# Optimization experiments

Measured on AMD Instinct MI355X. Metric: run time of the kernel, lower is better.

The kernel has to match this reference:

```python
import jax, jax.numpy as jnp
import numpy as np

N = 100000
E = 1600000
IN_C = 512
OUT_C = 128


def setup_inputs() -> dict:
    key = jax.random.key(0)
    k1, k2, k3, k4 = jax.random.split(key, 4)
    x = jax.random.normal(k1, (N, IN_C), dtype=jnp.float32)
    edge_index = jax.random.randint(k2, (2, E), 0, N, dtype=jnp.int64)
    # GCNConv parameters (glorot weight, zero bias as in PyG defaults)
    scale = jnp.sqrt(6.0 / (IN_C + OUT_C)).astype(jnp.float32)
    W = jax.random.uniform(k3, (IN_C, OUT_C), dtype=jnp.float32, minval=-scale, maxval=scale)
    b = jnp.zeros((OUT_C,), dtype=jnp.float32)
    return {"x": x, "edge_index": edge_index, "W": W, "b": b}


def reference(x, edge_index, W, b):
    n = x.shape[0]
    loops = jnp.arange(n, dtype=edge_index.dtype)
    src = jnp.concatenate([edge_index[0], loops])  # [E+N] message sources
    dst = jnp.concatenate([edge_index[1], loops])  # [E+N] message targets
    # symmetric GCN normalization: deg over targets incl. self-loops
    deg = jax.ops.segment_sum(jnp.ones_like(src, dtype=x.dtype), dst, num_segments=n)
    dinv = jnp.where(deg > 0, jax.lax.rsqrt(deg), 0.0)
    norm = dinv[src] * dinv[dst]  # [E+N]
    h = x @ W  # [N, OUT_C] transform first (in > out)
    msg = h[src] * norm[:, None]  # [E+N, OUT_C]
    out = jax.ops.segment_sum(msg, dst, num_segments=n) + b
    return (out, 0)
```

## Files before the change

kernel.cpp:

```cpp
#include <hip/hip_runtime.h>

#define IN_C 512
#define OUT_C 128
#define NB 128
#define CHUNK 16384

typedef float f32x4 __attribute__((ext_vector_type(4)));
typedef __bf16 bf16x8 __attribute__((ext_vector_type(8)));

static inline int cdiv(int a, int b) { return (a + b - 1) / b; }

__device__ __forceinline__ unsigned short bfbits(__bf16 h) {
  return __builtin_bit_cast(unsigned short, h);
}


__global__ __launch_bounds__(256) void hist_kernel(const int* __restrict__ dst,
                                                   int* __restrict__ table,
                                                   int nchunks, int E) {
  __shared__ int hcnt[NB];
  int t = threadIdx.x;
  int c = blockIdx.x;
  if (t < NB) hcnt[t] = 0;
  __syncthreads();
  int base = c * CHUNK;
  for (int i = t; i < CHUNK; i += 256) {
    int e = base + i;
    if (e < E) atomicAdd(&hcnt[dst[e] >> 10], 1);
  }
  __syncthreads();
  if (t < NB) table[t * nchunks + c] = hcnt[t];
}

__global__ __launch_bounds__(256) void tscan_kernel(int* __restrict__ table,
                                                    int* __restrict__ bstart,
                                                    int nchunks, int E) {
  __shared__ int sh[256];
  int t = threadIdx.x;
  int total = NB * nchunks;
  int S = (total + 255) / 256;
  int lo = t * S;
  int hi = lo + S; if (hi > total) hi = total;
  int s = 0;
  int i = lo;
  for (; i + 4 <= hi; i += 4)
    s += table[i] + table[i + 1] + table[i + 2] + table[i + 3];
  for (; i < hi; i++) s += table[i];
  sh[t] = s;
  __syncthreads();
  for (int off = 1; off < 256; off <<= 1) {
    int x = sh[t];
    if (t >= off) x += sh[t - off];
    __syncthreads();
    sh[t] = x;
    __syncthreads();
  }
  int run = sh[t] - s;
  for (i = lo; i < hi; i++) {
    int v = table[i];
    table[i] = run;
    run += v;
  }
  __syncthreads();
  for (int b = t; b < NB; b += 256) bstart[b] = table[b * nchunks];
  if (t == 0) bstart[NB] = E;
}

__global__ __launch_bounds__(256) void scat2_kernel(const int* __restrict__ src,
                                                    const int* __restrict__ dst,
                                                    const int* __restrict__ table,
                                                    int* __restrict__ inter,
                                                    int nchunks, int E) {
  __shared__ int cur[NB];
  int t = threadIdx.x;
  int c = blockIdx.x;
  if (t < NB) cur[t] = table[t * nchunks + c];
  __syncthreads();
  int base = c * CHUNK;
  for (int i = t; i < CHUNK; i += 256) {
    int e = base + i;
    if (e < E) {
      int d = dst[e];
      int pos = atomicAdd(&cur[d >> 10], 1);
      inter[pos] = (src[e] << 10) | (d & 1023);
    }
  }
}

__global__ __launch_bounds__(256) void bdeg_offs_kernel(const int* __restrict__ inter,
                                                        const int* __restrict__ bstart,
                                                        int* __restrict__ offs,
                                                        float* __restrict__ dinv,
                                                        int n, int E, int nbk) {
  __shared__ int dl[1024];
  __shared__ int sh[256];
  int t = threadIdx.x;
  int b = blockIdx.x;
  for (int i = t; i < 1024; i += 256) dl[i] = 0;
  __syncthreads();
  int lo = bstart[b], hi = bstart[b + 1];
  for (int e = lo + t; e < hi; e += 256) atomicAdd(&dl[inter[e] & 1023], 1);
  __syncthreads();
  int c[4];
  int s = 0;
#pragma unroll
  for (int j = 0; j < 4; j++) {
    c[j] = dl[t * 4 + j];
    s += c[j];
  }
  sh[t] = s;
  __syncthreads();
  for (int off = 1; off < 256; off <<= 1) {
    int x = sh[t];
    if (t >= off) x += sh[t - off];
    __syncthreads();
    sh[t] = x;
    __syncthreads();
  }
  int run = sh[t] - s + lo;
  int nb0 = b << 10;
#pragma unroll
  for (int j = 0; j < 4; j++) {
    int node = nb0 + t * 4 + j;
    if (node < n) {
      offs[node] = run;
      dinv[node] = rsqrtf((float)c[j] + 1.0f);
    }
    run += c[j];
  }
  if (b == nbk - 1 && t == 255) offs[n] = E;
}

__global__ __launch_bounds__(256) void scat3_kernel(const int* __restrict__ inter,
                                                    const int* __restrict__ bstart,
                                                    const int* __restrict__ offs,
                                                    int* __restrict__ csr_src, int n) {
  __shared__ int cur[1024];
  int t = threadIdx.x;
  int b = blockIdx.x;
  int nb0 = b << 10;
  for (int i = t; i < 1024; i += 256) {
    int node = nb0 + i;
    cur[i] = (node < n) ? offs[node] : 0;
  }
  __syncthreads();
  int lo = bstart[b], hi = bstart[b + 1];
  for (int e = lo + t; e < hi; e += 256) {
    int u = inter[e];
    int pos = atomicAdd(&cur[u & 1023], 1);
    csr_src[pos] = u >> 10;
  }
}

__global__ __launch_bounds__(256) void wsplit_kernel(const float* __restrict__ W,
                                                     unsigned short* __restrict__ wfh,
                                                     unsigned short* __restrict__ wfl) {
  int i = blockIdx.x * 256 + threadIdx.x;
  if (i >= IN_C * OUT_C) return;
  int k = i >> 7;
  int col = i & 127;
  float w = W[i];
  __bf16 hb = (__bf16)w;
  __bf16 lb = (__bf16)(w - (float)hb);
  int ks = k >> 5;
  int lg = (k & 31) >> 3;
  int j = k & 7;
  int cb = col >> 4;
  int lane = lg * 16 + (col & 15);
  size_t idx = ((size_t)(ks * 8 + cb) * 64 + lane) * 8 + j;
  wfh[idx] = bfbits(hb);
  wfl[idx] = bfbits(lb);
}

__global__ __launch_bounds__(256) void gemm_mfma_kernel(
    const float* __restrict__ x, const unsigned short* __restrict__ wfh,
    const unsigned short* __restrict__ wfl, const float* __restrict__ dinv,
    unsigned short* __restrict__ h, int n) {
  __shared__ float xs[2][4096];

  const int tid = threadIdx.x;
  const int wv = tid >> 6;
  const int lane = tid & 63;
  const int l15 = lane & 15;
  const int lg = lane >> 4;
  const int wr = wv >> 1;
  const int wc = wv & 1;
  const int row0 = blockIdx.x * 128;

  const float* gsrc[4];
#pragma unroll
  for (int i = 0; i < 4; i++) {
    int pslot = i * 256 + tid;
    int row = pslot >> 3;
    int q = pslot & 7;
    int s = q ^ (row & 7);
    int grow = row0 + row;
    if (grow > n - 1) grow = n - 1;
    gsrc[i] = x + (size_t)grow * IN_C + s * 4;
  }

  const unsigned short* bph = wfh + ((size_t)(wc * 4) * 64 + lane) * 8;
  const unsigned short* bpl = wfl + ((size_t)(wc * 4) * 64 + lane) * 8;

  f32x4 acc[4][4];
#pragma unroll
  for (int i = 0; i < 4; i++)
#pragma unroll
    for (int j = 0; j < 4; j++) acc[i][j] = (f32x4)0.0f;

#pragma unroll
  for (int i = 0; i < 4; i++) {
    char* lp = (char*)&xs[0][0] + i * 4096 + wv * 1024;
    __builtin_amdgcn_global_load_lds(
        (const __attribute__((address_space(1))) void*)gsrc[i],
        (__attribute__((address_space(3))) void*)lp, 16, 0, 0);
    gsrc[i] += 32;
  }

  for (int ks = 0; ks < 16; ks++) {
    __builtin_amdgcn_s_barrier();
    bf16x8 bh[4], bl[4];
#pragma unroll
    for (int nt = 0; nt < 4; nt++) {
      bh[nt] = __builtin_bit_cast(bf16x8, *(const uint4*)(bph + (size_t)ks * 4096 + nt * 512));
      bl[nt] = __builtin_bit_cast(bf16x8, *(const uint4*)(bpl + (size_t)ks * 4096 + nt * 512));
    }
    if (ks < 15) {
#pragma unroll
      for (int i = 0; i < 4; i++) {
        char* lp = (char*)&xs[(ks + 1) & 1][0] + i * 4096 + wv * 1024;
        __builtin_amdgcn_global_load_lds(
            (const __attribute__((address_space(1))) void*)gsrc[i],
            (__attribute__((address_space(3))) void*)lp, 16, 0, 0);
        gsrc[i] += 32;
      }
      asm volatile("s_waitcnt vmcnt(12)" ::: "memory");
    } else {
      asm volatile("s_waitcnt vmcnt(8)" ::: "memory");
    }
    __builtin_amdgcn_s_barrier();

    const float* bp = &xs[ks & 1][0];
    bf16x8 ah[4];
#pragma unroll
    for (int rt = 0; rt < 4; rt++) {
      int row = wr * 64 + rt * 16 + l15;
      int r7 = row & 7;
      int s0 = (lg * 2) ^ r7;
      int s1 = (lg * 2 + 1) ^ r7;
      float4 f0 = *(const float4*)(bp + row * 32 + s0 * 4);
      float4 f1 = *(const float4*)(bp + row * 32 + s1 * 4);
      float f[8] = {f0.x, f0.y, f0.z, f0.w, f1.x, f1.y, f1.z, f1.w};
      bf16x8 hh;
#pragma unroll
      for (int j = 0; j < 8; j++) hh[j] = (__bf16)f[j];
      ah[rt] = hh;
    }
#pragma unroll
    for (int rt = 0; rt < 4; rt++)
#pragma unroll
      for (int nt = 0; nt < 4; nt++) {
        acc[rt][nt] = __builtin_amdgcn_mfma_f32_16x16x32_bf16(ah[rt], bh[nt], acc[rt][nt], 0, 0, 0);
        acc[rt][nt] = __builtin_amdgcn_mfma_f32_16x16x32_bf16(ah[rt], bl[nt], acc[rt][nt], 0, 0, 0);
      }
  }

#pragma unroll
  for (int rt = 0; rt < 4; rt++) {
    int rowbase = row0 + wr * 64 + rt * 16 + lg * 4;
#pragma unroll
    for (int r = 0; r < 4; r++) {
      int row = rowbase + r;
      if (row < n) {
        float di = dinv[row];
#pragma unroll
        for (int nt = 0; nt < 4; nt++) {
          int col = wc * 64 + nt * 16 + l15;
          h[(size_t)row * OUT_C + col] = bfbits((__bf16)(acc[rt][nt][r] * di));
        }
      }
    }
  }
}

__device__ __forceinline__ float bflo(unsigned int u) {
  return __builtin_bit_cast(float, u << 16);
}
__device__ __forceinline__ float bfhi(unsigned int u) {
  return __builtin_bit_cast(float, u & 0xffff0000u);
}

__global__ __launch_bounds__(256) void gather_kernel(const int* __restrict__ offs,
                                                     const int* __restrict__ csr_src,
                                                     const unsigned short* __restrict__ h,
                                                     const float* __restrict__ dinv,
                                                     const float* __restrict__ b,
                                                     float* __restrict__ out,
                                                     int n, int tail) {
  int wid = threadIdx.x >> 6;
  int lane = threadIdx.x & 63;
  int l15 = lane & 15;
  int q = lane >> 4;
  int node = blockIdx.x * 4 + wid;
  if (node >= n) return;

  int start = offs[node];
  int end = offs[node + 1];

  float ax0 = 0, ay0 = 0, ax1 = 0, ay1 = 0, ax2 = 0, ay2 = 0, ax3 = 0, ay3 = 0;

  int e = start + q;
  for (; e + 12 < end; e += 16) {
    int s0 = csr_src[e];
    int s1 = csr_src[e + 4];
    int s2 = csr_src[e + 8];
    int s3 = csr_src[e + 12];
    uint4 u0 = *(const uint4*)(h + (size_t)s0 * OUT_C + l15 * 8);
    uint4 u1 = *(const uint4*)(h + (size_t)s1 * OUT_C + l15 * 8);
    uint4 u2 = *(const uint4*)(h + (size_t)s2 * OUT_C + l15 * 8);
    uint4 u3 = *(const uint4*)(h + (size_t)s3 * OUT_C + l15 * 8);
    ax0 += (bflo(u0.x) + bflo(u1.x)) + (bflo(u2.x) + bflo(u3.x));
    ay0 += (bfhi(u0.x) + bfhi(u1.x)) + (bfhi(u2.x) + bfhi(u3.x));
    ax1 += (bflo(u0.y) + bflo(u1.y)) + (bflo(u2.y) + bflo(u3.y));
    ay1 += (bfhi(u0.y) + bfhi(u1.y)) + (bfhi(u2.y) + bfhi(u3.y));
    ax2 += (bflo(u0.z) + bflo(u1.z)) + (bflo(u2.z) + bflo(u3.z));
    ay2 += (bfhi(u0.z) + bfhi(u1.z)) + (bfhi(u2.z) + bfhi(u3.z));
    ax3 += (bflo(u0.w) + bflo(u1.w)) + (bflo(u2.w) + bflo(u3.w));
    ay3 += (bfhi(u0.w) + bfhi(u1.w)) + (bfhi(u2.w) + bfhi(u3.w));
  }
  for (; e < end; e += 4) {
    int s0 = csr_src[e];
    uint4 u0 = *(const uint4*)(h + (size_t)s0 * OUT_C + l15 * 8);
    ax0 += bflo(u0.x); ay0 += bfhi(u0.x);
    ax1 += bflo(u0.y); ay1 += bfhi(u0.y);
    ax2 += bflo(u0.z); ay2 += bfhi(u0.z);
    ax3 += bflo(u0.w); ay3 += bfhi(u0.w);
  }

#pragma unroll
  for (int mask = 16; mask <= 32; mask <<= 1) {
    ax0 += __shfl_xor(ax0, mask); ay0 += __shfl_xor(ay0, mask);
    ax1 += __shfl_xor(ax1, mask); ay1 += __shfl_xor(ay1, mask);
    ax2 += __shfl_xor(ax2, mask); ay2 += __shfl_xor(ay2, mask);
    ax3 += __shfl_xor(ax3, mask); ay3 += __shfl_xor(ay3, mask);
  }

  float dd = dinv[node];
  uint4 us = *(const uint4*)(h + (size_t)node * OUT_C + l15 * 8);
  ax0 = (ax0 + bflo(us.x)) * dd; ay0 = (ay0 + bfhi(us.x)) * dd;
  ax1 = (ax1 + bflo(us.y)) * dd; ay1 = (ay1 + bfhi(us.y)) * dd;
  ax2 = (ax2 + bflo(us.z)) * dd; ay2 = (ay2 + bfhi(us.z)) * dd;
  ax3 = (ax3 + bflo(us.w)) * dd; ay3 = (ay3 + bfhi(us.w)) * dd;

  if (q == 0) {
    float4 b0 = *(const float4*)(b + l15 * 8);
    float4 b1 = *(const float4*)(b + l15 * 8 + 4);
    float4 o0 = make_float4(ax0 + b0.x, ay0 + b0.y, ax1 + b0.z, ay1 + b0.w);
    float4 o1 = make_float4(ax2 + b1.x, ay2 + b1.y, ax3 + b1.z, ay3 + b1.w);
    float* op = out + (size_t)node * OUT_C + l15 * 8;
    *(float4*)op = o0;
    *(float4*)(op + 4) = o1;
  }

  if (node == 0 && lane == 0) {
    for (int t = 0; t < tail; t++) out[(size_t)n * OUT_C + t] = 0.0f;
  }
}

extern "C" void kernel_launch(void* const* d_in, const int* in_sizes, int n_in,
                              void* d_out, int out_size, void* d_ws, size_t ws_size,
                              hipStream_t stream) {
  const float* x = (const float*)d_in[0];
  const int* ei = (const int*)d_in[1];
  const float* W = (const float*)d_in[2];
  const float* b = (const float*)d_in[3];

  const int n = in_sizes[0] / IN_C;
  const int E = in_sizes[1] / 2;
  const int* src = ei;
  const int* dst = ei + E;
  float* out = (float*)d_out;

  const int nchunks = cdiv(E, CHUNK);
  const int nbk = cdiv(n, 1024);

  size_t p = 0;
  auto alloc = [&](size_t bytes) { size_t o = p; p += (bytes + 255) & ~(size_t)255; return o; };
  char* ws = (char*)d_ws;
  float*          dinv   = (float*)(ws + alloc((size_t)n * 4));
  int*            offs   = (int*)(ws + alloc(((size_t)n + 1) * 4));
  int*            csrsrc = (int*)(ws + alloc((size_t)E * 4));
  int*            bstart = (int*)(ws + alloc((NB + 1) * 4));
  unsigned short* wfh    = (unsigned short*)(ws + alloc((size_t)IN_C * OUT_C * 2));
  unsigned short* wfl    = (unsigned short*)(ws + alloc((size_t)IN_C * OUT_C * 2));
  size_t upos = p;
  int*            inter  = (int*)(ws + upos);
  int*            table  = (int*)(ws + upos + (((size_t)E * 4 + 255) & ~(size_t)255));
  unsigned short* h      = (unsigned short*)(ws + upos);

  wsplit_kernel<<<cdiv(IN_C * OUT_C, 256), 256, 0, stream>>>(W, wfh, wfl);
  hist_kernel<<<nchunks, 256, 0, stream>>>(dst, table, nchunks, E);
  tscan_kernel<<<1, 256, 0, stream>>>(table, bstart, nchunks, E);
  scat2_kernel<<<nchunks, 256, 0, stream>>>(src, dst, table, inter, nchunks, E);
  bdeg_offs_kernel<<<nbk, 256, 0, stream>>>(inter, bstart, offs, dinv, n, E, nbk);
  scat3_kernel<<<nbk, 256, 0, stream>>>(inter, bstart, offs, csrsrc, n);
  gemm_mfma_kernel<<<cdiv(n, 128), 256, 0, stream>>>(x, wfh, wfl, dinv, h, n);
  int tail = out_size - n * OUT_C;
  gather_kernel<<<cdiv(n, 4), 256, 0, stream>>>(offs, csrsrc, h, dinv, b, out, n, tail);
}
```

Before: 281.3 us.

## Fuse bucket degree and CSR scatter kernels, simplify GEMM pipeline sync, halve chunk size

Merges the per-bucket degree/offset kernel with the CSR scatter kernel, so each bucket's running cursors stay in shared memory instead of being written to and reread from global memory, and one launch is dropped. Replaces the GEMM's explicit s_waitcnt/s_barrier double-buffer handshake with __syncthreads at the end of each k-step. This may serialize the prefetch more than the hand-tuned vmcnt waits did. Also halves CHUNK, which doubles the number of histogram/scatter blocks and enlarges the chunk table.

Result: faster. 264.7 us (-5.9%).

```diff
diff --git a/kernel.cpp b/kernel.cpp
--- a/kernel.cpp
+++ b/kernel.cpp
@@ -3,7 +3,7 @@
 #define IN_C 512
 #define OUT_C 128
 #define NB 128
-#define CHUNK 16384
+#define CHUNK 8192
 
 typedef float f32x4 __attribute__((ext_vector_type(4)));
 typedef __bf16 bf16x8 __attribute__((ext_vector_type(8)));
@@ -87,12 +87,14 @@
   }
 }
 
-__global__ __launch_bounds__(256) void bdeg_offs_kernel(const int* __restrict__ inter,
-                                                        const int* __restrict__ bstart,
-                                                        int* __restrict__ offs,
-                                                        float* __restrict__ dinv,
-                                                        int n, int E, int nbk) {
+__global__ __launch_bounds__(256) void bucket_csr_kernel(const int* __restrict__ inter,
+                                                         const int* __restrict__ bstart,
+                                                         int* __restrict__ offs,
+                                                         float* __restrict__ dinv,
+                                                         int* __restrict__ csr_src,
+                                                         int n, int E, int nbk) {
   __shared__ int dl[1024];
+  __shared__ int curs[1024];
   __shared__ int sh[256];
   int t = threadIdx.x;
   int b = blockIdx.x;
@@ -126,28 +128,14 @@
       offs[node] = run;
       dinv[node] = rsqrtf((float)c[j] + 1.0f);
     }
+    curs[t * 4 + j] = run;
     run += c[j];
   }
   if (b == nbk - 1 && t == 255) offs[n] = E;
-}
-
-__global__ __launch_bounds__(256) void scat3_kernel(const int* __restrict__ inter,
-                                                    const int* __restrict__ bstart,
-                                                    const int* __restrict__ offs,
-                                                    int* __restrict__ csr_src, int n) {
-  __shared__ int cur[1024];
-  int t = threadIdx.x;
-  int b = blockIdx.x;
-  int nb0 = b << 10;
-  for (int i = t; i < 1024; i += 256) {
-    int node = nb0 + i;
-    cur[i] = (node < n) ? offs[node] : 0;
-  }
-  __syncthreads();
-  int lo = bstart[b], hi = bstart[b + 1];
+  __syncthreads();
   for (int e = lo + t; e < hi; e += 256) {
     int u = inter[e];
-    int pos = atomicAdd(&cur[u & 1023], 1);
+    int pos = atomicAdd(&curs[u & 1023], 1);
     csr_src[pos] = u >> 10;
   }
 }
@@ -216,31 +204,27 @@
         (__attribute__((address_space(3))) void*)lp, 16, 0, 0);
     gsrc[i] += 32;
   }
-
+  __syncthreads();
+
+  int cur = 0;
   for (int ks = 0; ks < 16; ks++) {
-    __builtin_amdgcn_s_barrier();
-    bf16x8 bh[4], bl[4];
-#pragma unroll
-    for (int nt = 0; nt < 4; nt++) {
-      bh[nt] = __builtin_bit_cast(bf16x8, *(const uint4*)(bph + (size_t)ks * 4096 + nt * 512));
-      bl[nt] = __builtin_bit_cast(bf16x8, *(const uint4*)(bpl + (size_t)ks * 4096 + nt * 512));
-    }
     if (ks < 15) {
 #pragma unroll
       for (int i = 0; i < 4; i++) {
-        char* lp = (char*)&xs[(ks + 1) & 1][0] + i * 4096 + wv * 1024;
+        char* lp = (char*)&xs[cur ^ 1][0] + i * 4096 + wv * 1024;
         __builtin_amdgcn_global_load_lds(
             (const __attribute__((address_space(1))) void*)gsrc[i],
             (__attribute__((address_space(3))) void*)lp, 16, 0, 0);
         gsrc[i] += 32;
       }
-      asm volatile("s_waitcnt vmcnt(12)" ::: "memory");
-    } else {
-      asm volatile("s_waitcnt vmcnt(8)" ::: "memory");
-    }
-    __builtin_amdgcn_s_barrier();
-
-    const float* bp = &xs[ks & 1][0];
+    }
+    bf16x8 bh[4], bl[4];
+#pragma unroll
+    for (int nt = 0; nt < 4; nt++) {
+      bh[nt] = __builtin_bit_cast(bf16x8, *(const uint4*)(bph + (size_t)ks * 4096 + nt * 512));
+      bl[nt] = __builtin_bit_cast(bf16x8, *(const uint4*)(bpl + (size_t)ks * 4096 + nt * 512));
+    }
+    const float* bp = &xs[cur][0];
     bf16x8 ah[4];
 #pragma unroll
     for (int rt = 0; rt < 4; rt++) {
@@ -263,6 +247,8 @@
         acc[rt][nt] = __builtin_amdgcn_mfma_f32_16x16x32_bf16(ah[rt], bh[nt], acc[rt][nt], 0, 0, 0);
         acc[rt][nt] = __builtin_amdgcn_mfma_f32_16x16x32_bf16(ah[rt], bl[nt], acc[rt][nt], 0, 0, 0);
       }
+    __syncthreads();
+    cur ^= 1;
   }
 
 #pragma unroll
@@ -402,8 +388,7 @@
   hist_kernel<<<nchunks, 256, 0, stream>>>(dst, table, nchunks, E);
   tscan_kernel<<<1, 256, 0, stream>>>(table, bstart, nchunks, E);
   scat2_kernel<<<nchunks, 256, 0, stream>>>(src, dst, table, inter, nchunks, E);
-  bdeg_offs_kernel<<<nbk, 256, 0, stream>>>(inter, bstart, offs, dinv, n, E, nbk);
-  scat3_kernel<<<nbk, 256, 0, stream>>>(inter, bstart, offs, csrsrc, n);
+  bucket_csr_kernel<<<nbk, 256, 0, stream>>>(inter, bstart, offs, dinv, csrsrc, n, E, nbk);
   gemm_mfma_kernel<<<cdiv(n, 128), 256, 0, stream>>>(x, wfh, wfl, dinv, h, n);
   int tail = out_size - n * OUT_C;
   gather_kernel<<<cdiv(n, 4), 256, 0, stream>>>(offs, csrsrc, h, dinv, b, out, n, tail);
```
